# Optimization experiments

Measured on AMD Instinct MI355X. Metric: run time of the kernel, lower is better.

## Reference

```python
import jax, jax.numpy as jnp
import numpy as np

B, S, D, H = 1, 512, 128, 128
EPS = 1e-5


def layernorm(x, g, b):
    mu = jnp.mean(x, axis=-1, keepdims=True)
    var = jnp.mean(jnp.square(x - mu), axis=-1, keepdims=True)
    return (x - mu) * jax.lax.rsqrt(var + EPS) * g + b


def setup_inputs() -> dict:
    key = jax.random.key(0)
    ks = jax.random.split(key, 10)
    scale_d = 1.0 / np.sqrt(D)
    scale_h = 1.0 / np.sqrt(H)
    return {
        "x": jax.random.normal(ks[0], (B, S, S, D), dtype=jnp.float32),
        "mask": jax.random.uniform(ks[1], (B, S, S), dtype=jnp.float32),
        "norm_g": jnp.ones((D,), jnp.float32),
        "norm_b": jnp.zeros((D,), jnp.float32),
        "Wl": jax.random.normal(ks[2], (H, D), jnp.float32) * scale_d,
        "Wr": jax.random.normal(ks[3], (H, D), jnp.float32) * scale_d,
        "Wlg": jax.random.normal(ks[4], (H, D), jnp.float32) * scale_d,
        "Wrg": jax.random.normal(ks[5], (H, D), jnp.float32) * scale_d,
        "Wog": jax.random.normal(ks[6], (H, D), jnp.float32) * scale_d,
        "out_norm_g": jnp.ones((H,), jnp.float32),
        "out_norm_b": jnp.zeros((H,), jnp.float32),
        "Wout": jax.random.normal(ks[7], (D, H), jnp.float32) * scale_h,
    }


def reference(x, mask, norm_g, norm_b, Wl, Wr, Wlg, Wrg, Wog, out_norm_g, out_norm_b, Wout):
    # x: [B,S,S,D], mask: [B,S,S]
    xn = layernorm(x, norm_g, norm_b)
    m = mask[..., None]  # [B,S,S,1]
    left = (xn @ Wl.T) * m * jax.nn.sigmoid(xn @ Wlg.T)   # [B,S,S,H]
    right = (xn @ Wr.T) * m * jax.nn.sigmoid(xn @ Wrg.T)  # [B,S,S,H]
    out_gate = jax.nn.sigmoid(xn @ Wog.T)                  # [B,S,S,H]
    # per-channel triangular contraction over k
    out = jnp.einsum('bikd,bjkd->bijd', left, right)       # [B,S,S,H]
    out = layernorm(out, out_norm_g, out_norm_b) * out_gate
    return out @ Wout.T  # [B,S,S,D]
```

## Files before the change

kernel.cpp:

```cpp
#include <hip/hip_runtime.h>
#include <hip/hip_bf16.h>
#include <cstdint>

typedef unsigned short u16;
typedef unsigned int   u32;
typedef __bf16 bf16x8 __attribute__((ext_vector_type(8)));
typedef float  f32x4  __attribute__((ext_vector_type(4)));

#define S_    512
#define D_    128
#define H_    128
#define NPOS_ (S_ * S_)
#define LN_EPS 1e-5f

__device__ __forceinline__ u16 f2bf(float f) {
  union { __hip_bfloat16 h; u16 u; } cv;
  cv.h = __float2bfloat16(f);
  return cv.u;
}
__device__ __forceinline__ float bflo(u32 p) { return __uint_as_float(p << 16); }
__device__ __forceinline__ float bfhi(u32 p) { return __uint_as_float(p & 0xffff0000u); }
__device__ __forceinline__ float sigmoidf_(float x) { return 1.f / (1.f + __expf(-x)); }

__device__ __forceinline__ void gld16(const void* g, void* l) {
  __builtin_amdgcn_global_load_lds(
      (const __attribute__((address_space(1))) void*)g,
      (__attribute__((address_space(3))) void*)l, 16, 0, 0);
}

template <int CPR, int TOTAL>
__device__ __forceinline__ void stage_tile(const char* gbase, int ld_bytes, char* lds, int tid) {
#pragma unroll
  for (int c = tid; c < TOTAL; c += 256) {
    int row = c / CPR;
    int col = c - row * CPR;
    gld16(gbase + (size_t)row * ld_bytes + (size_t)col * 16, lds + (size_t)c * 16);
  }
}

__global__ __launch_bounds__(256) void k_prep(
    const float* __restrict__ wl, const float* __restrict__ wlg,
    const float* __restrict__ wr, const float* __restrict__ wrg,
    const float* __restrict__ wog, const float* __restrict__ wout,
    u16* __restrict__ wb) {
  int i = blockIdx.x * 256 + threadIdx.x;
  int m = i >> 14, o = i & 16383;
  const float* src = (m == 0) ? wl : (m == 1) ? wlg : (m == 2) ? wr
                   : (m == 3) ? wrg : (m == 4) ? wog : wout;
  wb[i] = f2bf(src[o]);
}

__device__ __forceinline__ void proj_k128(
    const u16* __restrict__ Wm, const u16* __restrict__ Wg,
    const u16* Xs, int wr, int wc, int quad, int lq,
    f32x4 acc0[4][4], f32x4 acc1[4][4]) {
#pragma unroll
  for (int ks = 0; ks < 4; ++ks) {
    const int kc = ks * 4 + quad;
    bf16x8 b[4], am[4], ag[4];
#pragma unroll
    for (int ni = 0; ni < 4; ++ni) {
      const int br = wc * 64 + ni * 16 + lq;
      b[ni] = *(const bf16x8*)((const char*)Xs + br * 256 + ((kc ^ (br & 15)) << 4));
    }
#pragma unroll
    for (int mi = 0; mi < 4; ++mi) {
      const int ar = wr * 64 + mi * 16 + lq;
      am[mi] = *(const bf16x8*)&Wm[(size_t)ar * D_ + kc * 8];
      if (Wg) ag[mi] = *(const bf16x8*)&Wg[(size_t)ar * D_ + kc * 8];
    }
#pragma unroll
    for (int mi = 0; mi < 4; ++mi)
#pragma unroll
      for (int ni = 0; ni < 4; ++ni) {
        acc0[mi][ni] = __builtin_amdgcn_mfma_f32_16x16x32_bf16(am[mi], b[ni], acc0[mi][ni], 0, 0, 0);
        if (Wg)
          acc1[mi][ni] = __builtin_amdgcn_mfma_f32_16x16x32_bf16(ag[mi], b[ni], acc1[mi][ni], 0, 0, 0);
      }
  }
}

__global__ __launch_bounds__(256, 2) void k_lnproj(
    const float* __restrict__ x, const float* __restrict__ mask,
    const float* __restrict__ ng, const float* __restrict__ nb,
    const u16* __restrict__ wb, u16* __restrict__ left_t,
    u16* __restrict__ right_t, u16* __restrict__ gate_t) {
  __shared__ u16 Xs[128 * 128];
  const int tid = threadIdx.x, w = tid >> 6, l = tid & 63;
  const int r0 = blockIdx.x * 128;
  const int half = l >> 5, lh = l & 31;

  {
    const float4 gg = ((const float4*)ng)[lh];
    const float4 bb = ((const float4*)nb)[lh];
#pragma unroll 4
    for (int it = 0; it < 16; ++it) {
      const int rr = it * 8 + w * 2 + half;
      float4 v = ((const float4*)(x + (size_t)(r0 + rr) * D_))[lh];
      float s = v.x + v.y + v.z + v.w;
      float q = v.x * v.x + v.y * v.y + v.z * v.z + v.w * v.w;
#pragma unroll
      for (int off = 16; off >= 1; off >>= 1) {
        s += __shfl_xor(s, off);
        q += __shfl_xor(q, off);
      }
      const float mu  = s * (1.f / 128.f);
      const float var = q * (1.f / 128.f) - mu * mu;
      const float rs  = rsqrtf(var + LN_EPS);
      const u32 p0 = (u32)f2bf((v.x - mu) * rs * gg.x + bb.x)
                   | ((u32)f2bf((v.y - mu) * rs * gg.y + bb.y) << 16);
      const u32 p1 = (u32)f2bf((v.z - mu) * rs * gg.z + bb.z)
                   | ((u32)f2bf((v.w - mu) * rs * gg.w + bb.w) << 16);
      u32* d = (u32*)((char*)Xs + rr * 256 + ((((lh >> 1)) ^ (rr & 15)) << 4) + ((lh & 1) << 3));
      d[0] = p0;
      d[1] = p1;
    }
  }
  __syncthreads();

  const int wr = w >> 1, wc = w & 1, quad = l >> 4, lq = l & 15;
  const f32x4 vz = {0.f, 0.f, 0.f, 0.f};
  f32x4 acc0[4][4], acc1[4][4];

#pragma unroll
  for (int g = 0; g < 2; ++g) {
    const u16* Wm = wb + (size_t)(2 * g) * (H_ * D_);
    const u16* Wg = wb + (size_t)(2 * g + 1) * (H_ * D_);
    u16* dst = g ? right_t : left_t;
#pragma unroll
    for (int i = 0; i < 4; ++i)
#pragma unroll
      for (int j = 0; j < 4; ++j) { acc0[i][j] = vz; acc1[i][j] = vz; }

    proj_k128(Wm, Wg, Xs, wr, wc, quad, lq, acc0, acc1);

#pragma unroll
    for (int ni = 0; ni < 4; ++ni) {
      const int r = r0 + wc * 64 + ni * 16 + lq;
      const float mk = mask[r];
#pragma unroll
      for (int mi = 0; mi < 4; ++mi)
#pragma unroll
        for (int reg = 0; reg < 4; ++reg) {
          const int hrow = wr * 64 + mi * 16 + quad * 4 + reg;
          dst[(size_t)hrow * NPOS_ + r] =
              f2bf(acc0[mi][ni][reg] * mk * sigmoidf_(acc1[mi][ni][reg]));
        }
    }
  }

#pragma unroll
  for (int i = 0; i < 4; ++i)
#pragma unroll
    for (int j = 0; j < 4; ++j) acc0[i][j] = vz;

  proj_k128(wb + (size_t)4 * (H_ * D_), (const u16*)nullptr, Xs, wr, wc, quad, lq, acc0, acc1);

#pragma unroll
  for (int ni = 0; ni < 4; ++ni) {
    const int r = r0 + wc * 64 + ni * 16 + lq;
#pragma unroll
    for (int mi = 0; mi < 4; ++mi)
#pragma unroll
      for (int reg = 0; reg < 4; ++reg) {
        const int hrow = wr * 64 + mi * 16 + quad * 4 + reg;
        gate_t[(size_t)hrow * NPOS_ + r] = f2bf(sigmoidf_(acc0[mi][ni][reg]));
      }
  }
}

__global__ __launch_bounds__(256, 2) void k_einsum(
    const u16* __restrict__ left_t, const u16* __restrict__ right_t,
    u16* __restrict__ out_t) {
  const int d = blockIdx.x;
  const int t = blockIdx.y;
  const int i0 = (t >> 2) * 128, j0 = (t & 3) * 128;
  __shared__ u16 As[128 * 64], Bs[128 * 64];
  const u16* L = left_t + (size_t)d * NPOS_;
  const u16* R = right_t + (size_t)d * NPOS_;
  const int tid = threadIdx.x;
  const int w = tid >> 6, l = tid & 63;
  const int wr = w >> 1, wc = w & 1;

  const f32x4 vz = {0.f, 0.f, 0.f, 0.f};
  f32x4 acc[4][4];
#pragma unroll
  for (int i = 0; i < 4; ++i)
#pragma unroll
    for (int j = 0; j < 4; ++j) acc[i][j] = vz;

  for (int kt = 0; kt < 8; ++kt) {
    stage_tile<8, 1024>((const char*)L + ((size_t)i0 * S_ + kt * 64) * 2, S_ * 2, (char*)As, tid);
    stage_tile<8, 1024>((const char*)R + ((size_t)j0 * S_ + kt * 64) * 2, S_ * 2, (char*)Bs, tid);
    __syncthreads();
#pragma unroll
    for (int kk = 0; kk < 2; ++kk) {
      const int ko = kk * 32 + (l >> 4) * 8;
      bf16x8 a[4], b[4];
#pragma unroll
      for (int mi = 0; mi < 4; ++mi)
        a[mi] = *(const bf16x8*)&As[(wr * 64 + mi * 16 + (l & 15)) * 64 + ko];
#pragma unroll
      for (int ni = 0; ni < 4; ++ni)
        b[ni] = *(const bf16x8*)&Bs[(wc * 64 + ni * 16 + (l & 15)) * 64 + ko];
#pragma unroll
      for (int mi = 0; mi < 4; ++mi)
#pragma unroll
        for (int ni = 0; ni < 4; ++ni)
          acc[mi][ni] = __builtin_amdgcn_mfma_f32_16x16x32_bf16(a[mi], b[ni], acc[mi][ni], 0, 0, 0);
    }
    __syncthreads();
  }

  const int quad = l >> 4, lc = l & 15;
  u16* O = out_t + (size_t)d * NPOS_;
#pragma unroll
  for (int mi = 0; mi < 4; ++mi)
#pragma unroll
    for (int ni = 0; ni < 4; ++ni) {
      const int col = j0 + wc * 64 + ni * 16 + lc;
#pragma unroll
      for (int reg = 0; reg < 4; ++reg) {
        const int row = i0 + wr * 64 + mi * 16 + quad * 4 + reg;
        O[(size_t)row * S_ + col] = f2bf(acc[mi][ni][reg]);
      }
    }
}

__global__ __launch_bounds__(256, 2) void k_final(
    const u16* __restrict__ out_t, const u16* __restrict__ gate_t,
    const float* __restrict__ og, const float* __restrict__ ob,
    const u16* __restrict__ wout_b, float* __restrict__ out) {
  __shared__ u16 A_lds[128 * 136];
  __shared__ u16 Wlds[128 * 128];
  __shared__ float psum[4][128], pq[4][128];
  __shared__ float mu_s[128], rs_s[128];
  const int tid = threadIdx.x, w = tid >> 6, l = tid & 63;
  const int r0 = blockIdx.x * 128;

  stage_tile<16, 2048>((const char*)wout_b, 256, (char*)Wlds, tid);

  float s0 = 0.f, s1 = 0.f, q0 = 0.f, q1 = 0.f;
  for (int it = 0; it < 32; ++it) {
    int d = it * 4 + w;
    u32 p = *(const u32*)&out_t[(size_t)d * NPOS_ + r0 + 2 * l];
    float f0 = bflo(p), f1 = bfhi(p);
    s0 += f0; s1 += f1; q0 += f0 * f0; q1 += f1 * f1;
  }
  psum[w][2 * l] = s0; psum[w][2 * l + 1] = s1;
  pq[w][2 * l] = q0;   pq[w][2 * l + 1] = q1;
  __syncthreads();
  if (tid < 128) {
    float s = psum[0][tid] + psum[1][tid] + psum[2][tid] + psum[3][tid];
    float q = pq[0][tid] + pq[1][tid] + pq[2][tid] + pq[3][tid];
    float mu  = s * (1.f / 128.f);
    float var = q * (1.f / 128.f) - mu * mu;
    mu_s[tid] = mu;
    rs_s[tid] = rsqrtf(var + LN_EPS);
  }
  __syncthreads();

  for (int it = 0; it < 32; ++it) {
    int d = it * 4 + w;
    u32 p  = *(const u32*)&out_t[(size_t)d * NPOS_ + r0 + 2 * l];
    u32 gp = *(const u32*)&gate_t[(size_t)d * NPOS_ + r0 + 2 * l];
    float gd = og[d], bd = ob[d];
    float f0 = bflo(p), f1 = bfhi(p);
    float g0 = bflo(gp), g1 = bfhi(gp);
    int ja = 2 * l, jb = 2 * l + 1;
    float a0 = ((f0 - mu_s[ja]) * rs_s[ja] * gd + bd) * g0;
    float a1 = ((f1 - mu_s[jb]) * rs_s[jb] * gd + bd) * g1;
    A_lds[(size_t)ja * 136 + d] = f2bf(a0);
    A_lds[(size_t)jb * 136 + d] = f2bf(a1);
  }
  __syncthreads();

  const int wr = w >> 1, wc = w & 1;
  const f32x4 vz = {0.f, 0.f, 0.f, 0.f};
  f32x4 acc[4][4];
#pragma unroll
  for (int i = 0; i < 4; ++i)
#pragma unroll
    for (int j = 0; j < 4; ++j) acc[i][j] = vz;
#pragma unroll
  for (int kk = 0; kk < 4; ++kk) {
    const int ko = kk * 32 + (l >> 4) * 8;
    bf16x8 a[4], b[4];
#pragma unroll
    for (int mi = 0; mi < 4; ++mi)
      a[mi] = *(const bf16x8*)&A_lds[(wr * 64 + mi * 16 + (l & 15)) * 136 + ko];
#pragma unroll
    for (int ni = 0; ni < 4; ++ni)
      b[ni] = *(const bf16x8*)&Wlds[(wc * 64 + ni * 16 + (l & 15)) * 128 + ko];
#pragma unroll
    for (int mi = 0; mi < 4; ++mi)
#pragma unroll
      for (int ni = 0; ni < 4; ++ni)
        acc[mi][ni] = __builtin_amdgcn_mfma_f32_16x16x32_bf16(a[mi], b[ni], acc[mi][ni], 0, 0, 0);
  }
  const int quad = l >> 4, lc = l & 15;
#pragma unroll
  for (int mi = 0; mi < 4; ++mi)
#pragma unroll
    for (int ni = 0; ni < 4; ++ni) {
      const int dout = wc * 64 + ni * 16 + lc;
#pragma unroll
      for (int reg = 0; reg < 4; ++reg) {
        const int row = r0 + wr * 64 + mi * 16 + quad * 4 + reg;
        out[(size_t)row * D_ + dout] = acc[mi][ni][reg];
      }
    }
}

extern "C" void kernel_launch(void* const* d_in, const int* in_sizes, int n_in,
                              void* d_out, int out_size, void* d_ws, size_t ws_size,
                              hipStream_t stream) {
  const float* x    = (const float*)d_in[0];
  const float* mask = (const float*)d_in[1];
  const float* ng   = (const float*)d_in[2];
  const float* nb   = (const float*)d_in[3];
  const float* Wl   = (const float*)d_in[4];
  const float* Wr   = (const float*)d_in[5];
  const float* Wlg  = (const float*)d_in[6];
  const float* Wrg  = (const float*)d_in[7];
  const float* Wog  = (const float*)d_in[8];
  const float* og   = (const float*)d_in[9];
  const float* ob   = (const float*)d_in[10];
  const float* Wout = (const float*)d_in[11];
  float* out = (float*)d_out;

  const size_t SLAB = (size_t)NPOS_ * H_ * 2;
  char* ws = (char*)d_ws;
  u16* left_t  = (u16*)(ws + SLAB);
  u16* right_t = (u16*)(ws + 2 * SLAB);
  u16* gate_t  = (u16*)(ws + 3 * SLAB);
  u16* wb      = (u16*)(ws + 4 * SLAB);
  u16* out_t   = (u16*)(ws);
  if (ws_size < 4 * SLAB + 6 * H_ * D_ * sizeof(u16)) return;

  k_prep<<<384, 256, 0, stream>>>(Wl, Wlg, Wr, Wrg, Wog, Wout, wb);
  k_lnproj<<<2048, 256, 0, stream>>>(x, mask, ng, nb, wb, left_t, right_t, gate_t);
  k_einsum<<<dim3(128, 16), 256, 0, stream>>>(left_t, right_t, out_t);
  k_final<<<2048, 256, 0, stream>>>(out_t, gate_t, og, ob, wb + 5 * H_ * D_, out);
}
```

Measured before the change: 476.0 us.

## Swizzle LDS tiles and stage transposed outputs through LDS for coalesced stores

XOR-swizzles the 16-byte chunks in the LDS tiles that feed the MFMA loads in the einsum and final kernels, to remove LDS bank conflicts. The lnproj and einsum epilogues now write results into a swizzled LDS tile and then flush it with 16-byte vector global stores, replacing scattered 2-byte stores. This costs extra LDS in lnproj (a second 32KB buffer, which may reduce occupancy) and extra barriers.

```diff
diff --git a/kernel.cpp b/kernel.cpp
--- a/kernel.cpp
+++ b/kernel.cpp
@@ -28,13 +28,14 @@
       (__attribute__((address_space(3))) void*)l, 16, 0, 0);
 }
 
-template <int CPR, int TOTAL>
+template <int CPR, int TOTAL, int SWZ>
 __device__ __forceinline__ void stage_tile(const char* gbase, int ld_bytes, char* lds, int tid) {
 #pragma unroll
   for (int c = tid; c < TOTAL; c += 256) {
     int row = c / CPR;
     int col = c - row * CPR;
-    gld16(gbase + (size_t)row * ld_bytes + (size_t)col * 16, lds + (size_t)c * 16);
+    int scol = col ^ (row & SWZ);
+    gld16(gbase + (size_t)row * ld_bytes + (size_t)scol * 16, lds + (size_t)c * 16);
   }
 }
 
@@ -80,12 +81,27 @@
   }
 }
 
+__device__ __forceinline__ void ts_put(u16* T, int row, int col, u16 v) {
+  *(u16*)((char*)T + row * 256 + ((((col >> 3) ^ (row & 15)) << 4) | ((col & 7) << 1))) = v;
+}
+
+__device__ __forceinline__ void ts_flush(const u16* T, u16* dst, size_t ld, size_t c0, int tid) {
+#pragma unroll
+  for (int it = 0; it < 8; ++it) {
+    const int c = it * 256 + tid;
+    const int row = c >> 4, cc = c & 15;
+    bf16x8 v = *(const bf16x8*)((const char*)T + row * 256 + ((cc ^ (row & 15)) << 4));
+    *(bf16x8*)&dst[(size_t)row * ld + c0 + cc * 8] = v;
+  }
+}
+
 __global__ __launch_bounds__(256, 2) void k_lnproj(
     const float* __restrict__ x, const float* __restrict__ mask,
     const float* __restrict__ ng, const float* __restrict__ nb,
     const u16* __restrict__ wb, u16* __restrict__ left_t,
     u16* __restrict__ right_t, u16* __restrict__ gate_t) {
   __shared__ u16 Xs[128 * 128];
+  __shared__ u16 Ts[128 * 128];
   const int tid = threadIdx.x, w = tid >> 6, l = tid & 63;
   const int r0 = blockIdx.x * 128;
   const int half = l >> 5, lh = l & 31;
@@ -136,17 +152,19 @@
 
 #pragma unroll
     for (int ni = 0; ni < 4; ++ni) {
-      const int r = r0 + wc * 64 + ni * 16 + lq;
-      const float mk = mask[r];
+      const int rc = wc * 64 + ni * 16 + lq;
+      const float mk = mask[r0 + rc];
 #pragma unroll
       for (int mi = 0; mi < 4; ++mi)
 #pragma unroll
         for (int reg = 0; reg < 4; ++reg) {
           const int hrow = wr * 64 + mi * 16 + quad * 4 + reg;
-          dst[(size_t)hrow * NPOS_ + r] =
-              f2bf(acc0[mi][ni][reg] * mk * sigmoidf_(acc1[mi][ni][reg]));
+          ts_put(Ts, hrow, rc, f2bf(acc0[mi][ni][reg] * mk * sigmoidf_(acc1[mi][ni][reg])));
         }
     }
+    __syncthreads();
+    ts_flush(Ts, dst, NPOS_, r0, tid);
+    __syncthreads();
   }
 
 #pragma unroll
@@ -158,15 +176,17 @@
 
 #pragma unroll
   for (int ni = 0; ni < 4; ++ni) {
-    const int r = r0 + wc * 64 + ni * 16 + lq;
+    const int rc = wc * 64 + ni * 16 + lq;
 #pragma unroll
     for (int mi = 0; mi < 4; ++mi)
 #pragma unroll
       for (int reg = 0; reg < 4; ++reg) {
         const int hrow = wr * 64 + mi * 16 + quad * 4 + reg;
-        gate_t[(size_t)hrow * NPOS_ + r] = f2bf(sigmoidf_(acc0[mi][ni][reg]));
-      }
-  }
+        ts_put(Ts, hrow, rc, f2bf(sigmoidf_(acc0[mi][ni][reg])));
+      }
+  }
+  __syncthreads();
+  ts_flush(Ts, gate_t, NPOS_, r0, tid);
 }
 
 __global__ __launch_bounds__(256, 2) void k_einsum(
@@ -175,12 +195,14 @@
   const int d = blockIdx.x;
   const int t = blockIdx.y;
   const int i0 = (t >> 2) * 128, j0 = (t & 3) * 128;
-  __shared__ u16 As[128 * 64], Bs[128 * 64];
+  __shared__ u16 SM[128 * 128];
+  u16* As = SM;
+  u16* Bs = SM + 128 * 64;
   const u16* L = left_t + (size_t)d * NPOS_;
   const u16* R = right_t + (size_t)d * NPOS_;
   const int tid = threadIdx.x;
   const int w = tid >> 6, l = tid & 63;
-  const int wr = w >> 1, wc = w & 1;
+  const int wr = w >> 1, wc = w & 1, quad = l >> 4, lq = l & 15;
 
   const f32x4 vz = {0.f, 0.f, 0.f, 0.f};
   f32x4 acc[4][4];
@@ -190,19 +212,23 @@
     for (int j = 0; j < 4; ++j) acc[i][j] = vz;
 
   for (int kt = 0; kt < 8; ++kt) {
-    stage_tile<8, 1024>((const char*)L + ((size_t)i0 * S_ + kt * 64) * 2, S_ * 2, (char*)As, tid);
-    stage_tile<8, 1024>((const char*)R + ((size_t)j0 * S_ + kt * 64) * 2, S_ * 2, (char*)Bs, tid);
+    stage_tile<8, 1024, 7>((const char*)L + ((size_t)i0 * S_ + kt * 64) * 2, S_ * 2, (char*)As, tid);
+    stage_tile<8, 1024, 7>((const char*)R + ((size_t)j0 * S_ + kt * 64) * 2, S_ * 2, (char*)Bs, tid);
     __syncthreads();
 #pragma unroll
     for (int kk = 0; kk < 2; ++kk) {
-      const int ko = kk * 32 + (l >> 4) * 8;
+      const int cs = kk * 4 + quad;
       bf16x8 a[4], b[4];
 #pragma unroll
-      for (int mi = 0; mi < 4; ++mi)
-        a[mi] = *(const bf16x8*)&As[(wr * 64 + mi * 16 + (l & 15)) * 64 + ko];
-#pragma unroll
-      for (int ni = 0; ni < 4; ++ni)
-        b[ni] = *(const bf16x8*)&Bs[(wc * 64 + ni * 16 + (l & 15)) * 64 + ko];
+      for (int mi = 0; mi < 4; ++mi) {
+        const int row = wr * 64 + mi * 16 + lq;
+        a[mi] = *(const bf16x8*)((const char*)As + row * 128 + ((cs ^ (row & 7)) << 4));
+      }
+#pragma unroll
+      for (int ni = 0; ni < 4; ++ni) {
+        const int row = wc * 64 + ni * 16 + lq;
+        b[ni] = *(const bf16x8*)((const char*)Bs + row * 128 + ((cs ^ (row & 7)) << 4));
+      }
 #pragma unroll
       for (int mi = 0; mi < 4; ++mi)
 #pragma unroll
@@ -212,19 +238,21 @@
     __syncthreads();
   }
 
-  const int quad = l >> 4, lc = l & 15;
-  u16* O = out_t + (size_t)d * NPOS_;
+  u16* T = SM;
 #pragma unroll
   for (int mi = 0; mi < 4; ++mi)
 #pragma unroll
     for (int ni = 0; ni < 4; ++ni) {
-      const int col = j0 + wc * 64 + ni * 16 + lc;
+      const int jc = wc * 64 + ni * 16 + lq;
 #pragma unroll
       for (int reg = 0; reg < 4; ++reg) {
-        const int row = i0 + wr * 64 + mi * 16 + quad * 4 + reg;
-        O[(size_t)row * S_ + col] = f2bf(acc[mi][ni][reg]);
-      }
-    }
+        const int row = wr * 64 + mi * 16 + quad * 4 + reg;
+        ts_put(T, row, jc, f2bf(acc[mi][ni][reg]));
+      }
+    }
+  __syncthreads();
+  u16* O = out_t + (size_t)d * NPOS_ + (size_t)i0 * S_;
+  ts_flush(T, O, S_, j0, tid);
 }
 
 __global__ __launch_bounds__(256, 2) void k_final(
@@ -238,7 +266,7 @@
   const int tid = threadIdx.x, w = tid >> 6, l = tid & 63;
   const int r0 = blockIdx.x * 128;
 
-  stage_tile<16, 2048>((const char*)wout_b, 256, (char*)Wlds, tid);
+  stage_tile<16, 2048, 15>((const char*)wout_b, 256, (char*)Wlds, tid);
 
   float s0 = 0.f, s1 = 0.f, q0 = 0.f, q1 = 0.f;
   for (int it = 0; it < 32; ++it) {
@@ -275,7 +303,7 @@
   }
   __syncthreads();
 
-  const int wr = w >> 1, wc = w & 1;
+  const int wr = w >> 1, wc = w & 1, quad = l >> 4, lq = l & 15;
   const f32x4 vz = {0.f, 0.f, 0.f, 0.f};
   f32x4 acc[4][4];
 #pragma unroll
@@ -284,21 +312,24 @@
     for (int j = 0; j < 4; ++j) acc[i][j] = vz;
 #pragma unroll
   for (int kk = 0; kk < 4; ++kk) {
-    const int ko = kk * 32 + (l >> 4) * 8;
+    const int ko = kk * 32 + quad * 8;
+    const int cs = kk * 4 + quad;
     bf16x8 a[4], b[4];
 #pragma unroll
     for (int mi = 0; mi < 4; ++mi)
-      a[mi] = *(const bf16x8*)&A_lds[(wr * 64 + mi * 16 + (l & 15)) * 136 + ko];
-#pragma unroll
-    for (int ni = 0; ni < 4; ++ni)
-      b[ni] = *(const bf16x8*)&Wlds[(wc * 64 + ni * 16 + (l & 15)) * 128 + ko];
+      a[mi] = *(const bf16x8*)&A_lds[(wr * 64 + mi * 16 + lq) * 136 + ko];
+#pragma unroll
+    for (int ni = 0; ni < 4; ++ni) {
+      const int row = wc * 64 + ni * 16 + lq;
+      b[ni] = *(const bf16x8*)((const char*)Wlds + row * 256 + ((cs ^ (row & 15)) << 4));
+    }
 #pragma unroll
     for (int mi = 0; mi < 4; ++mi)
 #pragma unroll
       for (int ni = 0; ni < 4; ++ni)
         acc[mi][ni] = __builtin_amdgcn_mfma_f32_16x16x32_bf16(a[mi], b[ni], acc[mi][ni], 0, 0, 0);
   }
-  const int quad = l >> 4, lc = l & 15;
+  const int lc = lq;
 #pragma unroll
   for (int mi = 0; mi < 4; ++mi)
 #pragma unroll
```

Measured after the change: 489.9 us. 2.9% more time.
